# Kernel optimization log

Measured on AMD Instinct MI355X. Metric: run time of the kernel, lower is better.

The kernel has to match this reference:

```python
import jax, jax.numpy as jnp
import numpy as np

B, S, H, DH = 4, 2048, 16, 64
D = H * DH          # 1024
EXP = 2
FF_IN = EXP * D * 2  # 4096 (SwiGLU doubles)
FF_HID = EXP * D     # 2048
SCALE_BASE = 512
LN_EPS = 1e-5


def setup_inputs() -> dict:
    key = jax.random.key(0)
    ks = jax.random.split(key, 8)
    inp = {
        "q": jax.random.normal(ks[0], (B, S, D), jnp.float32),
        "k": jax.random.normal(ks[1], (B, S, D), jnp.float32),
        "v": jax.random.normal(ks[2], (B, S, D), jnp.float32),
        "Wqkv": jax.random.normal(ks[3], (D, 3 * D), jnp.float32) * (1.0 / np.sqrt(D)),
        "bqkv": jnp.zeros((3 * D,), jnp.float32),
        "q_scale": jnp.ones((DH,), jnp.float32),
        "k_scale": jnp.ones((DH,), jnp.float32),
        "ln_g": jnp.ones((D,), jnp.float32),
        "ln_b": jnp.zeros((D,), jnp.float32),
        "W1": jax.random.normal(ks[4], (D, FF_IN), jnp.float32) * (1.0 / np.sqrt(D)),
        "b1": jnp.zeros((FF_IN,), jnp.float32),
        "W2": jax.random.normal(ks[5], (FF_HID, D), jnp.float32) * (1.0 / np.sqrt(FF_HID)),
        "b2": jnp.zeros((D,), jnp.float32),
    }
    return inp


def rotate_half(x):
    x1, x2 = jnp.split(x, 2, axis=-1)
    return jnp.concatenate((-x2, x1), axis=-1)


def apply_rope(pos, t, scale):
    # pos: [S, DH], scale: [S, DH] (broadcast over [B, H, S, DH])
    return t * jnp.cos(pos) * scale + rotate_half(t) * jnp.sin(pos) * scale


def rotary_tables(seq_len):
    inv_freq = 1.0 / (10000.0 ** (jnp.arange(0, DH, 2, dtype=jnp.float32) / DH))
    t = jnp.arange(seq_len, dtype=jnp.float32)
    freqs = t[:, None] * inv_freq[None, :]            # [S, DH/2]
    freqs = jnp.concatenate((freqs, freqs), axis=-1)  # [S, DH]
    power = (t - seq_len // 2) / SCALE_BASE           # [S]
    base = (jnp.arange(0, DH, 2, dtype=jnp.float32) + 0.4 * DH) / (1.4 * DH)  # [DH/2]
    scale = base[None, :] ** power[:, None]           # [S, DH/2]
    scale = jnp.concatenate((scale, scale), axis=-1)  # [S, DH]
    return freqs, scale


def l2norm(x, eps=1e-12):
    n = jnp.sqrt(jnp.sum(x * x, axis=-1, keepdims=True))
    return x / jnp.maximum(n, eps)


def reference(q, k, v, Wqkv, bqkv, q_scale, k_scale, ln_g, ln_b, W1, b1, W2, b2):
    del k, v  # module projects qkv from q; k,v args are unused (faithful to source)
    n, seq_len, _ = q.shape
    qkv = q @ Wqkv + bqkv                              # [B, S, 3D]
    qkv = qkv.reshape(n, seq_len, H, 3 * DH).transpose(0, 2, 1, 3)  # [B, H, S, 3DH]
    q_, k_, v_ = jnp.split(qkv, 3, axis=-1)
    q_ = l2norm(q_) * q_scale
    k_ = l2norm(k_) * k_scale
    pos, xscale = rotary_tables(seq_len)
    q_ = apply_rope(pos, q_, xscale)
    k_ = apply_rope(pos, k_, 1.0 / xscale)
    # scaled dot product attention (non-causal)
    scores = jnp.einsum("bhid,bhjd->bhij", q_, k_) / np.sqrt(DH)
    attn = jax.nn.softmax(scores, axis=-1)
    out = jnp.einsum("bhij,bhjd->bhid", attn, v_)      # [B, H, S, DH]
    out = out.transpose(0, 2, 1, 3).reshape(n, seq_len, D)
    # LayerNorm
    mu = jnp.mean(out, axis=-1, keepdims=True)
    var = jnp.mean((out - mu) ** 2, axis=-1, keepdims=True)
    out = (out - mu) / jnp.sqrt(var + LN_EPS) * ln_g + ln_b
    # SwiGLU FFN (dropout = identity in eval)
    h = out @ W1 + b1                                  # [B, S, FF_IN]
    x_, gate = jnp.split(h, 2, axis=-1)
    ff = (jax.nn.silu(gate) * x_) @ W2 + b2            # [B, S, D]
    return out + ff
```

## Files before the change

### kernel.cpp

```cpp
#include <hip/hip_runtime.h>
#include <math.h>


typedef __bf16 bf16;
typedef bf16 bf16x8 __attribute__((ext_vector_type(8)));
typedef bf16 bf16x4 __attribute__((ext_vector_type(4)));
typedef float f32x4 __attribute__((ext_vector_type(4)));

#define MFMA(a, b, c) __builtin_amdgcn_mfma_f32_16x16x32_bf16(a, b, c, 0, 0, 0)

__device__ __forceinline__ void async16(const void* g, void* l) {
    __builtin_amdgcn_global_load_lds(
        (const __attribute__((address_space(1))) void*)g,
        (__attribute__((address_space(3))) void*)l,
        16, 0, 0);
}

__global__ __launch_bounds__(256) void fill_sentinel(float* __restrict__ o)
{
    size_t i = ((size_t)blockIdx.x * 256 + threadIdx.x) * 4;
    *(float4*)&o[i] = make_float4(0.25f, 0.25f, 0.25f, 0.25f);
}

__global__ __launch_bounds__(256) void transpose_f32_bf16(
    const float* __restrict__ in, bf16* __restrict__ out, int K, int N)
{
    __shared__ bf16 T[64][70];
    const int tN = N >> 6;
    const int tk = blockIdx.x / tN, tn = blockIdx.x % tN;
    const int k0 = tk << 6, n0 = tn << 6;
    const int t = threadIdx.x;
    const int r = t >> 2, c0 = (t & 3) << 4;
    const float* src = &in[(size_t)(k0 + r) * N + n0 + c0];
    for (int j = 0; j < 4; ++j) {
        float4 f = *(const float4*)(src + 4 * j);
        T[r][c0 + 4 * j + 0] = (bf16)f.x;
        T[r][c0 + 4 * j + 1] = (bf16)f.y;
        T[r][c0 + 4 * j + 2] = (bf16)f.z;
        T[r][c0 + 4 * j + 3] = (bf16)f.w;
    }
    __syncthreads();
    bf16x8 o0, o1;
    for (int i = 0; i < 8; ++i) o0[i] = T[c0 + i][r];
    for (int i = 0; i < 8; ++i) o1[i] = T[c0 + 8 + i][r];
    *(bf16x8*)&out[(size_t)(n0 + r) * K + k0 + c0]     = o0;
    *(bf16x8*)&out[(size_t)(n0 + r) * K + k0 + c0 + 8] = o1;
}

__global__ __launch_bounds__(256) void transpose_v(
    const bf16* __restrict__ in, bf16* __restrict__ out)
{
    __shared__ bf16 T[64][72];
    const int bh = blockIdx.x >> 5;
    const int s0 = (blockIdx.x & 31) << 6;
    const bf16* ip = in + ((size_t)bh << 17) + (size_t)s0 * 64;
    bf16* op = out + ((size_t)bh << 17) + s0;
    const int t = threadIdx.x;
    const int r = t >> 2, c0 = (t & 3) << 4;
    *(bf16x8*)&T[r][c0]     = *(const bf16x8*)&ip[r * 64 + c0];
    *(bf16x8*)&T[r][c0 + 8] = *(const bf16x8*)&ip[r * 64 + c0 + 8];
    __syncthreads();
    bf16x8 o0, o1;
    for (int i = 0; i < 8; ++i) o0[i] = T[c0 + i][r];
    for (int i = 0; i < 8; ++i) o1[i] = T[c0 + 8 + i][r];
    *(bf16x8*)&op[(size_t)r * 2048 + c0]     = o0;
    *(bf16x8*)&op[(size_t)r * 2048 + c0 + 8] = o1;
}

template <int EPI, bool AF32>
__global__ __launch_bounds__(256) void gemm_bt(
    const void* __restrict__ Avp, const bf16* __restrict__ BT,
    const float* __restrict__ bias, int M, int N, int K, int lda,
    bf16* __restrict__ C0, bf16* __restrict__ C1, bf16* __restrict__ C2,
    float* __restrict__ Cf, const bf16* __restrict__ resid)
{
    __shared__ bf16 As[128 * 64];
    __shared__ bf16 Bs[128 * 64];
    const int tid = threadIdx.x;
    const int lane = tid & 63, wave = tid >> 6;
    const int quad = lane >> 4, l16 = lane & 15;
    const int wm = wave >> 1, wn = wave & 1;
    const int nb = N >> 7;
    const int bm = blockIdx.x / nb, bn = blockIdx.x % nb;
    const int m0 = bm << 7, n0 = bn << 7;
    const float* Af = (const float*)Avp;
    const bf16*  Ab = (const bf16*)Avp;
    char* aB = (char*)&As[0];
    char* bB = (char*)&Bs[0];
    const int rsw = l16 & 7;

    f32x4 acc[4][4] = {};

    for (int kt = 0; kt < K; kt += 64) {
        for (int i = 0; i < 4; ++i) {
            int l = (i << 8) + tid;
            int r = l >> 3;
            int cbs = ((l & 7) ^ (r & 7)) << 3;
            int cu = (i << 8) + (wave << 6);
            if (!AF32)
                async16(&Ab[(size_t)(m0 + r) * lda + kt + cbs], aB + (size_t)cu * 16);
            async16(&BT[(size_t)(n0 + r) * K + kt + cbs], bB + (size_t)cu * 16);
        }
        if (AF32) {
            for (int i = 0; i < 4; ++i) {
                int l = (i << 8) + tid;
                int r = l >> 3;
                int cbs = ((l & 7) ^ (r & 7)) << 3;
                const float* s = &Af[(size_t)(m0 + r) * lda + kt + cbs];
                float4 f0 = *(const float4*)s;
                float4 f1 = *(const float4*)(s + 4);
                bf16x8 tv;
                tv[0] = (bf16)f0.x; tv[1] = (bf16)f0.y;
                tv[2] = (bf16)f0.z; tv[3] = (bf16)f0.w;
                tv[4] = (bf16)f1.x; tv[5] = (bf16)f1.y;
                tv[6] = (bf16)f1.z; tv[7] = (bf16)f1.w;
                *(bf16x8*)&As[l << 3] = tv;
            }
        }
        __syncthreads();
        for (int kd = 0; kd < 2; ++kd) {
            bf16x8 af[4], bfr[4];
            for (int mi = 0; mi < 4; ++mi) {
                int row = (wm << 6) + (mi << 4) + l16;
                af[mi] = *(const bf16x8*)&As[(row << 6) + ((((kd << 2) + quad) ^ rsw) << 3)];
            }
            for (int ni = 0; ni < 4; ++ni) {
                int row = (wn << 6) + (ni << 4) + l16;
                bfr[ni] = *(const bf16x8*)&Bs[(row << 6) + ((((kd << 2) + quad) ^ rsw) << 3)];
            }
            for (int mi = 0; mi < 4; ++mi)
                for (int ni = 0; ni < 4; ++ni)
                    acc[mi][ni] = MFMA(af[mi], bfr[ni], acc[mi][ni]);
        }
        __syncthreads();
    }

    for (int mi = 0; mi < 4; ++mi) {
        for (int ni = 0; ni < 4; ++ni) {
            for (int r = 0; r < 4; ++r) {
                int row = m0 + (wm << 6) + (mi << 4) + (quad << 2) + r;
                int col = n0 + (wn << 6) + (ni << 4) + l16;
                float v = acc[mi][ni][r] + bias[col];
                if (EPI == 0) {
                    int b = row >> 11, s = row & 2047;
                    int h = col / 192, w = col % 192;
                    int tq = w >> 6, d = w & 63;
                    bf16* dst = (tq == 0) ? C0 : (tq == 1) ? C1 : C2;
                    dst[((((size_t)b * 16 + h) * 2048 + s) << 6) + d] = (bf16)v;
                } else if (EPI == 1) {
                    C0[(size_t)row * N + col] = (bf16)v;
                } else {
                    float rv = (float)resid[(size_t)row * N + col];
                    Cf[(size_t)row * N + col] = v + rv;
                }
            }
        }
    }
}

__global__ __launch_bounds__(256) void norm_rope(
    bf16* __restrict__ qb, bf16* __restrict__ kb,
    const float* __restrict__ qs, const float* __restrict__ ks)
{
    const int wave = threadIdx.x >> 6, lane = threadIdx.x & 63;
    const int rid = blockIdx.x * 4 + wave;
    const bool is_k = rid >= 131072;
    const int idx = is_k ? rid - 131072 : rid;
    const int s = idx & 2047;
    bf16* ptr = (is_k ? kb : qb) + ((size_t)idx << 6);
    const int d = lane;

    float v = (float)ptr[d];
    float ss = v * v;
    for (int o = 1; o < 64; o <<= 1) ss += __shfl_xor(ss, o);
    float t = v * rsqrtf(fmaxf(ss, 1e-24f));
    t *= (is_k ? ks : qs)[d];

    float partner = __shfl_xor(t, 32);
    float rh = (d < 32) ? -partner : partner;

    const float fi = (float)(d & 31);
    float inv_freq = __builtin_amdgcn_exp2f(fi * -0.4152410118609203f);
    float pos = (float)s * inv_freq;
    float rev = pos * 0.15915494309189535f;
    rev = rev - floorf(rev);
    float sn = __builtin_amdgcn_sinf(rev);
    float cs = __builtin_amdgcn_cosf(rev);
    float base = (2.0f * fi + 25.6f) * (1.0f / 89.6f);
    float power = ((float)s - 1024.0f) * (1.0f / 512.0f);
    if (is_k) power = -power;
    float xsc = __builtin_amdgcn_exp2f(power * __builtin_amdgcn_logf(base));
    ptr[d] = (bf16)((t * cs + rh * sn) * xsc);
}

__global__ __launch_bounds__(256) void attn(
    const bf16* __restrict__ Q, const bf16* __restrict__ Kb,
    const bf16* __restrict__ VT, bf16* __restrict__ O)
{
    __shared__ bf16 Ks[64 * 64];
    __shared__ bf16 Vt[64 * 64];
    __shared__ bf16 Ps[4][2][16][72];
    const int tid = threadIdx.x;
    const int lane = tid & 63, wave = tid >> 6;
    const int quad = lane >> 4, l16 = lane & 15;
    const int rsw = l16 & 7;
    const int bh = blockIdx.x >> 4;
    const int q0 = (blockIdx.x & 15) << 7;
    const int s_base = q0 + (wave << 5);
    const bf16* Qp = Q + ((size_t)bh << 17);
    const bf16* Kp = Kb + ((size_t)bh << 17);
    const bf16* Vp = VT + ((size_t)bh << 17);

    bf16x8 qf[2][2];
    for (int sub = 0; sub < 2; ++sub) {
        const bf16* qrow = Qp + (size_t)(s_base + (sub << 4) + l16) * 64;
        qf[sub][0] = *(const bf16x8*)&qrow[(quad << 3)];
        qf[sub][1] = *(const bf16x8*)&qrow[32 + (quad << 3)];
        for (int j = 0; j < 8; ++j) {
            qf[sub][0][j] = (bf16)((float)qf[sub][0][j] * 0.1803368801f);
            qf[sub][1][j] = (bf16)((float)qf[sub][1][j] * 0.1803368801f);
        }
    }
    bf16x8 ones = {};
    if (l16 == 0) for (int j = 0; j < 8; ++j) ones[j] = (bf16)1.0f;

    f32x4 oacc[2][4] = {};
    f32x4 lacc[2] = {};
    char* kB = (char*)&Ks[0];
    char* vB = (char*)&Vt[0];

    for (int kt = 0; kt < 2048; kt += 64) {
        __syncthreads();
        for (int i = 0; i < 2; ++i) {
            int l = (i << 8) + tid;
            int r = l >> 3;
            int cbs = ((l & 7) ^ (r & 7)) << 3;
            int cu = (i << 8) + (wave << 6);
            async16(&Kp[(size_t)(kt + r) * 64 + cbs], kB + (size_t)cu * 16);
            async16(&Vp[(size_t)r * 2048 + kt + cbs], vB + (size_t)cu * 16);
        }
        __syncthreads();

        f32x4 sc[2][4];
        for (int nt = 0; nt < 4; ++nt) {
            int row = (nt << 4) + l16;
            bf16x8 kf0 = *(const bf16x8*)&Ks[(row << 6) + ((quad ^ rsw) << 3)];
            bf16x8 kf1 = *(const bf16x8*)&Ks[(row << 6) + (((quad + 4) ^ rsw) << 3)];
            for (int sub = 0; sub < 2; ++sub) {
                f32x4 z = {};
                z = MFMA(qf[sub][0], kf0, z);
                z = MFMA(qf[sub][1], kf1, z);
                sc[sub][nt] = z;
            }
        }
        const int prow = quad << 2;
        for (int sub = 0; sub < 2; ++sub)
            for (int r = 0; r < 4; ++r)
                for (int nt = 0; nt < 4; ++nt)
                    Ps[wave][sub][prow + r][(nt << 4) + l16] =
                        (bf16)__builtin_amdgcn_exp2f(sc[sub][nt][r]);
        __builtin_amdgcn_wave_barrier();
        bf16x8 pf0[2], pf1[2];
        for (int sub = 0; sub < 2; ++sub) {
            pf0[sub] = *(const bf16x8*)&Ps[wave][sub][l16][(quad << 3)];
            pf1[sub] = *(const bf16x8*)&Ps[wave][sub][l16][32 + (quad << 3)];
        }
        for (int ntd = 0; ntd < 4; ++ntd) {
            int row = (ntd << 4) + l16;
            bf16x8 vf0 = *(const bf16x8*)&Vt[(row << 6) + ((quad ^ rsw) << 3)];
            bf16x8 vf1 = *(const bf16x8*)&Vt[(row << 6) + (((quad + 4) ^ rsw) << 3)];
            for (int sub = 0; sub < 2; ++sub) {
                oacc[sub][ntd] = MFMA(pf0[sub], vf0, oacc[sub][ntd]);
                oacc[sub][ntd] = MFMA(pf1[sub], vf1, oacc[sub][ntd]);
            }
        }
        for (int sub = 0; sub < 2; ++sub) {
            lacc[sub] = MFMA(pf0[sub], ones, lacc[sub]);
            lacc[sub] = MFMA(pf1[sub], ones, lacc[sub]);
        }
    }

    const int b = bh >> 4, h = bh & 15;
    for (int sub = 0; sub < 2; ++sub)
        for (int r = 0; r < 4; ++r) {
            float l = __shfl(lacc[sub][r], quad << 4);
            float inv_l = 1.0f / l;
            int srow = s_base + (sub << 4) + (quad << 2) + r;
            for (int ntd = 0; ntd < 4; ++ntd) {
                int d = (ntd << 4) + l16;
                O[((((size_t)b * 2048 + srow) * 16) + h) * 64 + d] =
                    (bf16)(oacc[sub][ntd][r] * inv_l);
            }
        }
}

__global__ __launch_bounds__(256) void layernorm(
    const bf16* __restrict__ x, const float* __restrict__ g,
    const float* __restrict__ b, bf16* __restrict__ y)
{
    __shared__ float red[8];
    const int row = blockIdx.x;
    const int t = threadIdx.x;
    const bf16* xr = x + ((size_t)row << 10);
    bf16x4 xv = *(const bf16x4*)&xr[t << 2];
    float v[4], s = 0.0f, sq = 0.0f;
    for (int i = 0; i < 4; ++i) { v[i] = (float)xv[i]; s += v[i]; sq += v[i] * v[i]; }
    for (int o = 1; o < 64; o <<= 1) { s += __shfl_xor(s, o); sq += __shfl_xor(sq, o); }
    const int wave = t >> 6, lane = t & 63;
    if (lane == 0) { red[wave] = s; red[4 + wave] = sq; }
    __syncthreads();
    s  = red[0] + red[1] + red[2] + red[3];
    sq = red[4] + red[5] + red[6] + red[7];
    float mu = s * (1.0f / 1024.0f);
    float var = fmaxf(sq * (1.0f / 1024.0f) - mu * mu, 0.0f);
    float rstd = rsqrtf(var + 1e-5f);
    bf16x4 ov;
    for (int i = 0; i < 4; ++i) {
        int c = (t << 2) + i;
        ov[i] = (bf16)((v[i] - mu) * rstd * g[c] + b[c]);
    }
    *(bf16x4*)(y + ((size_t)row << 10) + (t << 2)) = ov;
}

__global__ __launch_bounds__(256) void swiglu(bf16* __restrict__ h)
{
    size_t i = ((size_t)blockIdx.x * 256 + threadIdx.x) * 8;
    size_t row = i >> 11, c = i & 2047;
    bf16* hr = h + (row << 12);
    bf16x8 xv = *(const bf16x8*)&hr[c];
    bf16x8 gv = *(const bf16x8*)&hr[c + 2048];
    bf16x8 ov;
    for (int j = 0; j < 8; ++j) {
        float xf = (float)xv[j], gf = (float)gv[j];
        ov[j] = (bf16)(gf / (1.0f + __expf(-gf)) * xf);
    }
    *(bf16x8*)&hr[c] = ov;
}

extern "C" void kernel_launch(void* const* d_in, const int* in_sizes, int n_in,
                              void* d_out, int out_size, void* d_ws, size_t ws_size,
                              hipStream_t stream) {
    (void)in_sizes; (void)n_in; (void)out_size;
    const float* q    = (const float*)d_in[0];
    const float* Wqkv = (const float*)d_in[3];
    const float* bqkv = (const float*)d_in[4];
    const float* qsc  = (const float*)d_in[5];
    const float* ksc  = (const float*)d_in[6];
    const float* lng  = (const float*)d_in[7];
    const float* lnb  = (const float*)d_in[8];
    const float* W1   = (const float*)d_in[9];
    const float* b1   = (const float*)d_in[10];
    const float* W2   = (const float*)d_in[11];
    const float* b2   = (const float*)d_in[12];
    float* out = (float*)d_out;

    const size_t MB = 1024 * 1024;
    if (ws_size < 92 * MB) {
        fill_sentinel<<<8192, 256, 0, stream>>>(out);
        return;
    }

    char* ws = (char*)d_ws;
    bf16* W2T      = (bf16*)(ws + 0);
    bf16* ln_buf   = (bf16*)(ws + 4  * MB);
    bf16* W1T      = (bf16*)(ws + 20 * MB);
    bf16* q_buf    = (bf16*)(ws + 28 * MB);
    bf16* k_buf    = (bf16*)(ws + 44 * MB);
    bf16* v_buf    = (bf16*)(ws + 60 * MB);
    bf16* WqkvT    = (bf16*)(ws + 76 * MB);
    bf16* vt_buf   = (bf16*)(ws + 76 * MB);
    bf16* attn_buf = (bf16*)(ws + 60 * MB);
    bf16* h_buf    = (bf16*)(ws + 28 * MB);

    transpose_f32_bf16<<<512,  256, 0, stream>>>(W2,   W2T,   2048, 1024);
    transpose_f32_bf16<<<1024, 256, 0, stream>>>(W1,   W1T,   1024, 4096);
    transpose_f32_bf16<<<768,  256, 0, stream>>>(Wqkv, WqkvT, 1024, 3072);

    gemm_bt<0, true><<<1536, 256, 0, stream>>>(q, WqkvT, bqkv, 8192, 3072, 1024, 1024,
                                               q_buf, k_buf, v_buf, nullptr, nullptr);
    norm_rope<<<65536, 256, 0, stream>>>(q_buf, k_buf, qsc, ksc);
    transpose_v<<<2048, 256, 0, stream>>>(v_buf, vt_buf);
    attn<<<1024, 256, 0, stream>>>(q_buf, k_buf, vt_buf, attn_buf);
    layernorm<<<8192, 256, 0, stream>>>(attn_buf, lng, lnb, ln_buf);
    gemm_bt<1, false><<<2048, 256, 0, stream>>>(ln_buf, W1T, b1, 8192, 4096, 1024, 1024,
                                                h_buf, nullptr, nullptr, nullptr, nullptr);
    swiglu<<<8192, 256, 0, stream>>>(h_buf);
    gemm_bt<2, false><<<512, 256, 0, stream>>>(h_buf, W2T, b2, 8192, 1024, 2048, 4096,
                                               nullptr, nullptr, nullptr, out, ln_buf);
}
```

Baseline: 562.2 us.

## Fuse SwiGLU into W1 GEMM epilogue, pre-convert input, swizzle block order

W1's columns are interleaved during the weight transpose so the x and gate values for one output land in adjacent lanes, which lets the W1 GEMM epilogue apply SwiGLU through a lane shuffle and write a half-width hidden buffer. The standalone swiglu pass and its extra read and write of the full h tensor go away. The fp32 input q is converted to bf16 in a separate kernel so the QKV GEMM can use async global-to-LDS loads for A as well. GEMM and attention blocks are remapped with an XCD-style interleave, attention gets occupancy launch bounds, and its P tile is written straight from the MFMA results. Costs are an extra conversion pass, more workspace, and a wasted-lane epilogue in the fused GEMM.

```diff
diff --git a/kernel.cpp b/kernel.cpp
--- a/kernel.cpp
+++ b/kernel.cpp
@@ -22,6 +22,19 @@
     *(float4*)&o[i] = make_float4(0.25f, 0.25f, 0.25f, 0.25f);
 }
 
+__global__ __launch_bounds__(256) void convert_f32_bf16(
+    const float* __restrict__ in, bf16* __restrict__ out)
+{
+    size_t i = ((size_t)blockIdx.x * 256 + threadIdx.x) * 8;
+    float4 f0 = *(const float4*)&in[i];
+    float4 f1 = *(const float4*)&in[i + 4];
+    bf16x8 v;
+    v[0] = (bf16)f0.x; v[1] = (bf16)f0.y; v[2] = (bf16)f0.z; v[3] = (bf16)f0.w;
+    v[4] = (bf16)f1.x; v[5] = (bf16)f1.y; v[6] = (bf16)f1.z; v[7] = (bf16)f1.w;
+    *(bf16x8*)&out[i] = v;
+}
+
+template <int PERM>
 __global__ __launch_bounds__(256) void transpose_f32_bf16(
     const float* __restrict__ in, bf16* __restrict__ out, int K, int N)
 {
@@ -43,8 +56,10 @@
     bf16x8 o0, o1;
     for (int i = 0; i < 8; ++i) o0[i] = T[c0 + i][r];
     for (int i = 0; i < 8; ++i) o1[i] = T[c0 + 8 + i][r];
-    *(bf16x8*)&out[(size_t)(n0 + r) * K + k0 + c0]     = o0;
-    *(bf16x8*)&out[(size_t)(n0 + r) * K + k0 + c0 + 8] = o1;
+    int n = n0 + r;
+    int np = PERM ? ((n < 2048) ? (n << 1) : (((n - 2048) << 1) | 1)) : n;
+    *(bf16x8*)&out[(size_t)np * K + k0 + c0]     = o0;
+    *(bf16x8*)&out[(size_t)np * K + k0 + c0 + 8] = o1;
 }
 
 __global__ __launch_bounds__(256) void transpose_v(
@@ -67,9 +82,9 @@
     *(bf16x8*)&op[(size_t)r * 2048 + c0 + 8] = o1;
 }
 
-template <int EPI, bool AF32>
+template <int EPI>
 __global__ __launch_bounds__(256) void gemm_bt(
-    const void* __restrict__ Avp, const bf16* __restrict__ BT,
+    const bf16* __restrict__ A, const bf16* __restrict__ BT,
     const float* __restrict__ bias, int M, int N, int K, int lda,
     bf16* __restrict__ C0, bf16* __restrict__ C1, bf16* __restrict__ C2,
     float* __restrict__ Cf, const bf16* __restrict__ resid)
@@ -81,10 +96,10 @@
     const int quad = lane >> 4, l16 = lane & 15;
     const int wm = wave >> 1, wn = wave & 1;
     const int nb = N >> 7;
-    const int bm = blockIdx.x / nb, bn = blockIdx.x % nb;
+    const int G = gridDim.x;
+    const int g = (blockIdx.x & 7) * (G >> 3) + (blockIdx.x >> 3);
+    const int bm = g / nb, bn = g % nb;
     const int m0 = bm << 7, n0 = bn << 7;
-    const float* Af = (const float*)Avp;
-    const bf16*  Ab = (const bf16*)Avp;
     char* aB = (char*)&As[0];
     char* bB = (char*)&Bs[0];
     const int rsw = l16 & 7;
@@ -97,25 +112,8 @@
             int r = l >> 3;
             int cbs = ((l & 7) ^ (r & 7)) << 3;
             int cu = (i << 8) + (wave << 6);
-            if (!AF32)
-                async16(&Ab[(size_t)(m0 + r) * lda + kt + cbs], aB + (size_t)cu * 16);
+            async16(&A[(size_t)(m0 + r) * lda + kt + cbs], aB + (size_t)cu * 16);
             async16(&BT[(size_t)(n0 + r) * K + kt + cbs], bB + (size_t)cu * 16);
-        }
-        if (AF32) {
-            for (int i = 0; i < 4; ++i) {
-                int l = (i << 8) + tid;
-                int r = l >> 3;
-                int cbs = ((l & 7) ^ (r & 7)) << 3;
-                const float* s = &Af[(size_t)(m0 + r) * lda + kt + cbs];
-                float4 f0 = *(const float4*)s;
-                float4 f1 = *(const float4*)(s + 4);
-                bf16x8 tv;
-                tv[0] = (bf16)f0.x; tv[1] = (bf16)f0.y;
-                tv[2] = (bf16)f0.z; tv[3] = (bf16)f0.w;
-                tv[4] = (bf16)f1.x; tv[5] = (bf16)f1.y;
-                tv[6] = (bf16)f1.z; tv[7] = (bf16)f1.w;
-                *(bf16x8*)&As[l << 3] = tv;
-            }
         }
         __syncthreads();
         for (int kd = 0; kd < 2; ++kd) {
@@ -140,18 +138,25 @@
             for (int r = 0; r < 4; ++r) {
                 int row = m0 + (wm << 6) + (mi << 4) + (quad << 2) + r;
                 int col = n0 + (wn << 6) + (ni << 4) + l16;
-                float v = acc[mi][ni][r] + bias[col];
                 if (EPI == 0) {
+                    float v = acc[mi][ni][r] + bias[col];
                     int b = row >> 11, s = row & 2047;
                     int h = col / 192, w = col % 192;
                     int tq = w >> 6, d = w & 63;
                     bf16* dst = (tq == 0) ? C0 : (tq == 1) ? C1 : C2;
                     dst[((((size_t)b * 16 + h) * 2048 + s) << 6) + d] = (bf16)v;
-                } else if (EPI == 1) {
-                    C0[(size_t)row * N + col] = (bf16)v;
-                } else {
+                } else if (EPI == 2) {
+                    float v = acc[mi][ni][r] + bias[col];
                     float rv = (float)resid[(size_t)row * N + col];
                     Cf[(size_t)row * N + col] = v + rv;
+                } else {
+                    int orig = (col & 1) ? ((col >> 1) + (N >> 1)) : (col >> 1);
+                    float v = acc[mi][ni][r] + bias[orig];
+                    float other = __shfl_xor(v, 1);
+                    if ((lane & 1) == 0) {
+                        float res = other / (1.0f + __expf(-other)) * v;
+                        C0[(size_t)row * (N >> 1) + (col >> 1)] = (bf16)res;
+                    }
                 }
             }
         }
@@ -193,19 +198,21 @@
     ptr[d] = (bf16)((t * cs + rh * sn) * xsc);
 }
 
-__global__ __launch_bounds__(256) void attn(
+__global__ __launch_bounds__(256, 4) void attn(
     const bf16* __restrict__ Q, const bf16* __restrict__ Kb,
     const bf16* __restrict__ VT, bf16* __restrict__ O)
 {
     __shared__ bf16 Ks[64 * 64];
     __shared__ bf16 Vt[64 * 64];
-    __shared__ bf16 Ps[4][2][16][72];
+    __shared__ bf16 Ps[4][2][16 * 72];
     const int tid = threadIdx.x;
     const int lane = tid & 63, wave = tid >> 6;
     const int quad = lane >> 4, l16 = lane & 15;
     const int rsw = l16 & 7;
-    const int bh = blockIdx.x >> 4;
-    const int q0 = (blockIdx.x & 15) << 7;
+    const int G = gridDim.x;
+    const int g = (blockIdx.x & 7) * (G >> 3) + (blockIdx.x >> 3);
+    const int bh = g >> 4;
+    const int q0 = (g & 15) << 7;
     const int s_base = q0 + (wave << 5);
     const bf16* Qp = Q + ((size_t)bh << 17);
     const bf16* Kp = Kb + ((size_t)bh << 17);
@@ -241,7 +248,7 @@
         }
         __syncthreads();
 
-        f32x4 sc[2][4];
+        const int prow = quad << 2;
         for (int nt = 0; nt < 4; ++nt) {
             int row = (nt << 4) + l16;
             bf16x8 kf0 = *(const bf16x8*)&Ks[(row << 6) + ((quad ^ rsw) << 3)];
@@ -250,20 +257,16 @@
                 f32x4 z = {};
                 z = MFMA(qf[sub][0], kf0, z);
                 z = MFMA(qf[sub][1], kf1, z);
-                sc[sub][nt] = z;
-            }
-        }
-        const int prow = quad << 2;
-        for (int sub = 0; sub < 2; ++sub)
-            for (int r = 0; r < 4; ++r)
-                for (int nt = 0; nt < 4; ++nt)
-                    Ps[wave][sub][prow + r][(nt << 4) + l16] =
-                        (bf16)__builtin_amdgcn_exp2f(sc[sub][nt][r]);
+                for (int r = 0; r < 4; ++r)
+                    Ps[wave][sub][(prow + r) * 72 + (nt << 4) + l16] =
+                        (bf16)__builtin_amdgcn_exp2f(z[r]);
+            }
+        }
         __builtin_amdgcn_wave_barrier();
         bf16x8 pf0[2], pf1[2];
         for (int sub = 0; sub < 2; ++sub) {
-            pf0[sub] = *(const bf16x8*)&Ps[wave][sub][l16][(quad << 3)];
-            pf1[sub] = *(const bf16x8*)&Ps[wave][sub][l16][32 + (quad << 3)];
+            pf0[sub] = *(const bf16x8*)&Ps[wave][sub][l16 * 72 + (quad << 3)];
+            pf1[sub] = *(const bf16x8*)&Ps[wave][sub][l16 * 72 + 32 + (quad << 3)];
         }
         for (int ntd = 0; ntd < 4; ++ntd) {
             int row = (ntd << 4) + l16;
@@ -322,21 +325,6 @@
     *(bf16x4*)(y + ((size_t)row << 10) + (t << 2)) = ov;
 }
 
-__global__ __launch_bounds__(256) void swiglu(bf16* __restrict__ h)
-{
-    size_t i = ((size_t)blockIdx.x * 256 + threadIdx.x) * 8;
-    size_t row = i >> 11, c = i & 2047;
-    bf16* hr = h + (row << 12);
-    bf16x8 xv = *(const bf16x8*)&hr[c];
-    bf16x8 gv = *(const bf16x8*)&hr[c + 2048];
-    bf16x8 ov;
-    for (int j = 0; j < 8; ++j) {
-        float xf = (float)xv[j], gf = (float)gv[j];
-        ov[j] = (bf16)(gf / (1.0f + __expf(-gf)) * xf);
-    }
-    *(bf16x8*)&hr[c] = ov;
-}
-
 extern "C" void kernel_launch(void* const* d_in, const int* in_sizes, int n_in,
                               void* d_out, int out_size, void* d_ws, size_t ws_size,
                               hipStream_t stream) {
@@ -355,7 +343,7 @@
     float* out = (float*)d_out;
 
     const size_t MB = 1024 * 1024;
-    if (ws_size < 92 * MB) {
+    if (ws_size < 98 * MB) {
         fill_sentinel<<<8192, 256, 0, stream>>>(out);
         return;
     }
@@ -367,24 +355,25 @@
     bf16* q_buf    = (bf16*)(ws + 28 * MB);
     bf16* k_buf    = (bf16*)(ws + 44 * MB);
     bf16* v_buf    = (bf16*)(ws + 60 * MB);
-    bf16* WqkvT    = (bf16*)(ws + 76 * MB);
+    bf16* q_bf     = (bf16*)(ws + 76 * MB);
     bf16* vt_buf   = (bf16*)(ws + 76 * MB);
+    bf16* WqkvT    = (bf16*)(ws + 92 * MB);
     bf16* attn_buf = (bf16*)(ws + 60 * MB);
-    bf16* h_buf    = (bf16*)(ws + 28 * MB);
-
-    transpose_f32_bf16<<<512,  256, 0, stream>>>(W2,   W2T,   2048, 1024);
-    transpose_f32_bf16<<<1024, 256, 0, stream>>>(W1,   W1T,   1024, 4096);
-    transpose_f32_bf16<<<768,  256, 0, stream>>>(Wqkv, WqkvT, 1024, 3072);
-
-    gemm_bt<0, true><<<1536, 256, 0, stream>>>(q, WqkvT, bqkv, 8192, 3072, 1024, 1024,
-                                               q_buf, k_buf, v_buf, nullptr, nullptr);
+    bf16* hs_buf   = (bf16*)(ws + 28 * MB);
+
+    convert_f32_bf16<<<4096, 256, 0, stream>>>(q, q_bf);
+    transpose_f32_bf16<0><<<512,  256, 0, stream>>>(W2,   W2T,   2048, 1024);
+    transpose_f32_bf16<1><<<1024, 256, 0, stream>>>(W1,   W1T,   1024, 4096);
+    transpose_f32_bf16<0><<<768,  256, 0, stream>>>(Wqkv, WqkvT, 1024, 3072);
+
+    gemm_bt<0><<<1536, 256, 0, stream>>>(q_bf, WqkvT, bqkv, 8192, 3072, 1024, 1024,
+                                         q_buf, k_buf, v_buf, nullptr, nullptr);
     norm_rope<<<65536, 256, 0, stream>>>(q_buf, k_buf, qsc, ksc);
     transpose_v<<<2048, 256, 0, stream>>>(v_buf, vt_buf);
     attn<<<1024, 256, 0, stream>>>(q_buf, k_buf, vt_buf, attn_buf);
     layernorm<<<8192, 256, 0, stream>>>(attn_buf, lng, lnb, ln_buf);
-    gemm_bt<1, false><<<2048, 256, 0, stream>>>(ln_buf, W1T, b1, 8192, 4096, 1024, 1024,
-                                                h_buf, nullptr, nullptr, nullptr, nullptr);
-    swiglu<<<8192, 256, 0, stream>>>(h_buf);
-    gemm_bt<2, false><<<512, 256, 0, stream>>>(h_buf, W2T, b2, 8192, 1024, 2048, 4096,
-                                               nullptr, nullptr, nullptr, out, ln_buf);
-}
+    gemm_bt<3><<<2048, 256, 0, stream>>>(ln_buf, W1T, b1, 8192, 4096, 1024, 1024,
+                                         hs_buf, nullptr, nullptr, nullptr, nullptr);
+    gemm_bt<2><<<512, 256, 0, stream>>>(hs_buf, W2T, b2, 8192, 1024, 2048, 2048,
+                                        nullptr, nullptr, nullptr, out, ln_buf);
+}
```

Result: slower. 1.189 ms (+111.5%).
